# Optimization experiments

Measured on AMD Instinct MI355X. Metric: run time of the kernel, lower is better.

The kernel has to match this reference:

```python
import jax, jax.numpy as jnp
import numpy as np

LOG2PI = float(np.log(2.0 * np.pi))
CLIP_LO, CLIP_HI = 1e-6, 1.0 - 1e-6


def gaussian_log_prob(X, mu):
    # X: (s, d), mu: (K, d) -> (s, K); unit-variance diagonal Normal.
    d = X.shape[-1]
    sq = (
        (X * X).sum(-1, keepdims=True)
        - 2.0 * (X @ mu.T)
        + (mu * mu).sum(-1)[None, :]
    )
    return -0.5 * (sq + d * LOG2PI)


def setup_inputs() -> dict:
    key = jax.random.key(0)
    kz, ks, kd, km1, km2 = jax.random.split(key, 5)
    s, K, n, dz = 60000, 200, 6, 64
    Z = jax.random.normal(kz, (s, dz), dtype=jnp.float32)
    S = jax.random.normal(ks, (s, 3), dtype=jnp.float32)
    D = jax.random.randint(kd, (s, n), 0, s, dtype=jnp.int64)
    sel_mu = jax.random.normal(km1, (K, dz), dtype=jnp.float32)
    spa_mu = jax.random.normal(km2, (K, 3), dtype=jnp.float32)
    return {"Z": Z, "S": S, "D": D, "sel_mu": sel_mu, "spa_mu": spa_mu}


def reference(Z, S, D, sel_mu, spa_mu):
    # point energy U: (s, K)
    U = -(gaussian_log_prob(Z, sel_mu) + gaussian_log_prob(S, spa_mu))
    Q = jax.nn.softmax(-U, axis=-1)  # temperature = 1.0
    # expected point energy: (s,)
    point = (Q * U).sum(-1)
    # doublet energy: gather neighbor rows, coassignment, potential, mask
    Qc = jnp.clip(Q, CLIP_LO, CLIP_HI)
    co = jnp.einsum('snk,sk->sn', Qc[D], Qc)  # (s, n)
    doublet = jnp.where(D < 0, 0.0, -jnp.log(co)).sum(-1)  # (s,)
    return point + doublet
```

## Files before the change

### kernel.cpp

```cpp
#include <hip/hip_runtime.h>
#include <hip/hip_fp16.h>
#include <math.h>

#define KK 200
#define NT 13
#define NNB 6
#define Q8STRIDE 256

typedef __attribute__((ext_vector_type(8))) short short8;
typedef __attribute__((ext_vector_type(4))) float f32x4;
typedef _Float16 half2v __attribute__((ext_vector_type(2)));
typedef __fp16 fp16x2 __attribute__((ext_vector_type(2)));
#define MFMA16 __builtin_amdgcn_mfma_f32_16x16x32_bf16

union U8 { short8 s; uint4 u; };
union H2U { half2v h; unsigned u; };
union P2U { fp16x2 h; unsigned u; };

__device__ __forceinline__ unsigned short bfh(float f) {
    unsigned u = __float_as_uint(f);
    return (unsigned short)((u + 0x7fffu + ((u >> 16) & 1u)) >> 16);
}
__device__ __forceinline__ float bf2f(unsigned short h) {
    return __uint_as_float(((unsigned)h) << 16);
}
__device__ __forceinline__ short8 z8() {
    short8 v;
#pragma unroll
    for (int j = 0; j < 8; ++j) v[j] = 0;
    return v;
}
__device__ __forceinline__ void cvp(float f0, float f1, unsigned& hw, unsigned& lw) {
    unsigned u0 = __float_as_uint(f0), u1 = __float_as_uint(f1);
    float l0 = f0 - __uint_as_float(u0 & 0xffff0000u);
    float l1 = f1 - __uint_as_float(u1 & 0xffff0000u);
    hw = __builtin_amdgcn_perm(u1, u0, 0x07060302u);
    lw = __builtin_amdgcn_perm(__float_as_uint(l1), __float_as_uint(l0), 0x07060302u);
}
__device__ __forceinline__ unsigned e5pair_lo(unsigned w) {
    return __builtin_amdgcn_perm(w, 0u, 0x05000400u);
}
__device__ __forceinline__ unsigned e5pair_hi(unsigned w) {
    return __builtin_amdgcn_perm(w, 0u, 0x07000600u);
}
__device__ __forceinline__ half2v as_h2(unsigned u) { H2U x; x.u = u; return x.h; }
__device__ __forceinline__ unsigned pkrtz_u(float a, float b) {
    P2U x; x.h = __builtin_amdgcn_cvt_pkrtz(a, b); return x.u;
}

__global__ __launch_bounds__(512, 4) void
k_point(const float* __restrict__ Z, const float* __restrict__ S,
        const float* __restrict__ selmu, const float* __restrict__ spamu,
        unsigned char* __restrict__ Qc8, float* __restrict__ pointbuf,
        int sRows, int mTiles)
{
    __shared__ short8 ldsBh[26 * 64];
    __shared__ short8 ldsBl[26 * 64];
    __shared__ uint2  ldsB2h[NT * 16];
    __shared__ uint2  ldsB2l[NT * 16];
    __shared__ float  normAcc[NT * 16];

    const int tid = threadIdx.x;

    if (tid < NT * 16) normAcc[tid] = 0.f;
    __syncthreads();

    for (int slot = tid; slot < 26 * 64; slot += 512) {
        int L = slot & 63, ts = slot >> 6;
        int t = ts >> 1, sstep = ts & 1;
        int n = t * 16 + (L & 15);
        int kb = sstep * 32 + (L >> 4) * 8;
        U8 hi, lo;
        hi.s = z8(); lo.s = z8();
        if (n < KK) {
            const float* mp = selmu + (size_t)n * 64 + kb;
            float4 a = *(const float4*)mp;
            float4 b = *(const float4*)(mp + 4);
            cvp(a.x, a.y, hi.u.x, lo.u.x);
            cvp(a.z, a.w, hi.u.y, lo.u.y);
            cvp(b.x, b.y, hi.u.z, lo.u.z);
            cvp(b.z, b.w, hi.u.w, lo.u.w);
            float ss = a.x*a.x + a.y*a.y + a.z*a.z + a.w*a.w
                     + b.x*b.x + b.y*b.y + b.z*b.z + b.w*b.w;
            atomicAdd(&normAcc[n], ss);
        }
        ldsBh[slot] = hi.s;
        ldsBl[slot] = lo.s;
    }
    __syncthreads();
    if (tid < NT * 16) {
        int n = tid;
        uint2 vh = make_uint2(0, 0), vl = make_uint2(0, 0);
        if (n < KK) {
            float p0 = spamu[n * 3 + 0], p1 = spamu[n * 3 + 1], p2 = spamu[n * 3 + 2];
            float nrm = -0.5f * (normAcc[n] + p0 * p0 + p1 * p1 + p2 * p2);
            unsigned short h0 = bfh(p0), h1 = bfh(p1), h2 = bfh(p2), h3 = bfh(nrm);
            unsigned short g0 = bfh(p0 - bf2f(h0)), g1 = bfh(p1 - bf2f(h1));
            unsigned short g2 = bfh(p2 - bf2f(h2)), g3 = bfh(nrm - bf2f(h3));
            vh = make_uint2((unsigned)h0 | ((unsigned)h1 << 16), (unsigned)h2 | ((unsigned)h3 << 16));
            vl = make_uint2((unsigned)g0 | ((unsigned)g1 << 16), (unsigned)g2 | ((unsigned)g3 << 16));
        }
        ldsB2h[tid] = vh;
        ldsB2l[tid] = vl;
    }
    __syncthreads();

    const int wave = tid >> 6;
    const int lane = tid & 63;
    const int q = lane >> 4;
    const int li = lane & 15;
    const float cLog = 0.5f * 67.0f * 1.8378770664093453f;

    const int tile = blockIdx.x * 8 + wave;
    if (tile >= mTiles) return;
    const int m0 = tile * 16;
    const int row = m0 + li;
    const int rowA = (row < sRows) ? row : (sRows - 1);

    const float* zr = Z + (size_t)rowA * 64 + q * 8;
    float4 z0 = *(const float4*)zr;
    float4 z1 = *(const float4*)(zr + 4);
    float4 z2 = *(const float4*)(zr + 32);
    float4 z3 = *(const float4*)(zr + 36);
    U8 ah0, al0, ah1, al1;
    cvp(z0.x, z0.y, ah0.u.x, al0.u.x);
    cvp(z0.z, z0.w, ah0.u.y, al0.u.y);
    cvp(z1.x, z1.y, ah0.u.z, al0.u.z);
    cvp(z1.z, z1.w, ah0.u.w, al0.u.w);
    cvp(z2.x, z2.y, ah1.u.x, al1.u.x);
    cvp(z2.z, z2.w, ah1.u.y, al1.u.y);
    cvp(z3.x, z3.y, ah1.u.z, al1.u.z);
    cvp(z3.z, z3.w, ah1.u.w, al1.u.w);

    float zz = z0.x*z0.x + z0.y*z0.y + z0.z*z0.z + z0.w*z0.w
             + z1.x*z1.x + z1.y*z1.y + z1.z*z1.z + z1.w*z1.w
             + z2.x*z2.x + z2.y*z2.y + z2.z*z2.z + z2.w*z2.w
             + z3.x*z3.x + z3.y*z3.y + z3.z*z3.z + z3.w*z3.w;
    zz += __shfl_xor(zz, 16);
    zz += __shfl_xor(zz, 32);

    float s0v = S[(size_t)rowA * 3 + 0];
    float s1v = S[(size_t)rowA * 3 + 1];
    float s2v = S[(size_t)rowA * 3 + 2];
    float cz = 0.5f * (zz + s0v * s0v + s1v * s1v + s2v * s2v) + cLog;

    U8 rsh, rsl;
    rsh.s = z8(); rsl.s = z8();
    if (lane < 16) {
        cvp(s0v, s1v, rsh.u.x, rsl.u.x);
        unsigned hw, lw;
        cvp(s2v, 1.0f, hw, lw);
        rsh.u.y = hw;
        rsl.u.y = lw & 0x0000ffffu;
    }

    f32x4 acc[NT];
#pragma unroll
    for (int t = 0; t < NT; ++t) { f32x4 zv = {0.f, 0.f, 0.f, 0.f}; acc[t] = zv; }

#pragma unroll
    for (int t = 0; t < NT; ++t) {
        short8 b0 = ldsBh[(t * 2 + 0) * 64 + lane];
        short8 b1 = ldsBh[(t * 2 + 1) * 64 + lane];
        short8 c0 = ldsBl[(t * 2 + 0) * 64 + lane];
        short8 c1 = ldsBl[(t * 2 + 1) * 64 + lane];
        uint2 bh2 = make_uint2(0, 0), bl2 = make_uint2(0, 0);
        if (lane < 16) { bh2 = ldsB2h[t * 16 + lane]; bl2 = ldsB2l[t * 16 + lane]; }
        U8 cmh, cml;
        cmh.s = z8(); cml.s = z8();
        cmh.u.x = bh2.x; cmh.u.y = bh2.y;
        cml.u.x = bl2.x; cml.u.y = bl2.y;

        acc[t] = MFMA16(b0, ah0.s, acc[t], 0, 0, 0);
        acc[t] = MFMA16(b1, ah1.s, acc[t], 0, 0, 0);
        acc[t] = MFMA16(b0, al0.s, acc[t], 0, 0, 0);
        acc[t] = MFMA16(b1, al1.s, acc[t], 0, 0, 0);
        acc[t] = MFMA16(c0, ah0.s, acc[t], 0, 0, 0);
        acc[t] = MFMA16(c1, ah1.s, acc[t], 0, 0, 0);
        acc[t] = MFMA16(cmh.s, rsh.s, acc[t], 0, 0, 0);
        acc[t] = MFMA16(cmh.s, rsl.s, acc[t], 0, 0, 0);
        acc[t] = MFMA16(cml.s, rsh.s, acc[t], 0, 0, 0);
    }

    const bool padQ = (q >= 2);
    float mx = -1e30f;
#pragma unroll
    for (int t = 0; t < NT; ++t) {
#pragma unroll
        for (int r = 0; r < 4; ++r) {
            float v = acc[t][r];
            if (t == 12 && padQ) v = -1e30f;
            acc[t][r] = v;
            mx = fmaxf(mx, v);
        }
    }
    mx = fmaxf(mx, __shfl_xor(mx, 16));
    mx = fmaxf(mx, __shfl_xor(mx, 32));
    float sl = 0.f, pl = 0.f;
#pragma unroll
    for (int t = 0; t < NT; ++t) {
#pragma unroll
        for (int r = 0; r < 4; ++r) {
            float v = acc[t][r];
            float ee = __expf(v - mx);
            sl += ee;
            pl = fmaf(ee, v, pl);
            acc[t][r] = ee;
        }
    }
    sl += __shfl_xor(sl, 16);
    sl += __shfl_xor(sl, 32);
    pl += __shfl_xor(pl, 16);
    pl += __shfl_xor(pl, 32);
    float inv = 1.0f / sl;

    if (row < sRows) {
        unsigned char* qp = Qc8 + (size_t)row * Q8STRIDE + q * 4;
#pragma unroll
        for (int t = 0; t < NT; ++t) {
            unsigned w = 0;
            if (t < 12 || !padQ) {
                float c0 = fminf(fmaxf(acc[t][0] * inv, 1e-6f), 1.0f - 1e-6f) * 1024.0f;
                float c1 = fminf(fmaxf(acc[t][1] * inv, 1e-6f), 1.0f - 1e-6f) * 1024.0f;
                float c2 = fminf(fmaxf(acc[t][2] * inv, 1e-6f), 1.0f - 1e-6f) * 1024.0f;
                float c3 = fminf(fmaxf(acc[t][3] * inv, 1e-6f), 1.0f - 1e-6f) * 1024.0f;
                unsigned ua = pkrtz_u(c0, c1);
                unsigned ub = pkrtz_u(c2, c3);
                unsigned t0 = ua + 0x007f007fu + ((ua >> 8) & 0x00010001u);
                unsigned t1 = ub + 0x007f007fu + ((ub >> 8) & 0x00010001u);
                w = __builtin_amdgcn_perm(t1, t0, 0x07050301u);
            }
            *(unsigned*)(qp + t * 16) = w;
        }
        if (lane < 16) pointbuf[row] = cz - pl * inv;
    }
}

__global__ __launch_bounds__(512, 8) void
k_doublet(const unsigned char* __restrict__ Qc8, const float* __restrict__ pointbuf,
          const int* __restrict__ D, float* __restrict__ out, int sRows)
{
    const int wave = threadIdx.x >> 6;
    const int lane = threadIdx.x & 63;
    const int half = lane >> 5;
    const int l = lane & 31;
    const int row = blockIdx.x * 8 + wave;
    if (row >= sRows) return;

    const bool act = (l < 25);
    const int lc = act ? l : 0;
    const float LN2_20 = 13.862943611198906f;

    const int* dp = D + (size_t)row * NNB;
    int da0 = dp[0], da1 = dp[1], da2 = dp[2], da3 = dp[3], da4 = dp[4], da5 = dp[5];
    int dj[3];
    dj[0] = half ? da1 : da0;
    dj[1] = half ? da3 : da2;
    dj[2] = half ? da5 : da4;

    uint2 ow = *(const uint2*)(Qc8 + (size_t)row * Q8STRIDE + lc * 8);
    uint2 nb[3];
#pragma unroll
    for (int i = 0; i < 3; ++i) {
        int dd = (dj[i] >= 0) ? dj[i] : row;
        nb[i] = *(const uint2*)(Qc8 + (size_t)dd * Q8STRIDE + lc * 8);
    }

    unsigned o0 = e5pair_lo(ow.x), o1 = e5pair_hi(ow.x);
    unsigned o2 = e5pair_lo(ow.y), o3 = e5pair_hi(ow.y);

    float pj[3];
#pragma unroll
    for (int i = 0; i < 3; ++i) {
        unsigned b0 = e5pair_lo(nb[i].x), b1 = e5pair_hi(nb[i].x);
        unsigned b2 = e5pair_lo(nb[i].y), b3 = e5pair_hi(nb[i].y);
        float t = 0.f;
#if __has_builtin(__builtin_amdgcn_fdot2)
        t = __builtin_amdgcn_fdot2(as_h2(o0), as_h2(b0), t, false);
        t = __builtin_amdgcn_fdot2(as_h2(o1), as_h2(b1), t, false);
        t = __builtin_amdgcn_fdot2(as_h2(o2), as_h2(b2), t, false);
        t = __builtin_amdgcn_fdot2(as_h2(o3), as_h2(b3), t, false);
#else
        {
            half2v ov[4] = { as_h2(o0), as_h2(o1), as_h2(o2), as_h2(o3) };
            half2v bv[4] = { as_h2(b0), as_h2(b1), as_h2(b2), as_h2(b3) };
#pragma unroll
            for (int k = 0; k < 4; ++k) {
                t = fmaf((float)ov[k][0], (float)bv[k][0], t);
                t = fmaf((float)ov[k][1], (float)bv[k][1], t);
            }
        }
#endif
        pj[i] = act ? t : 0.f;
    }
#pragma unroll
    for (int off = 1; off <= 16; off <<= 1) {
#pragma unroll
        for (int i = 0; i < 3; ++i) pj[i] += __shfl_xor(pj[i], off);
    }
    float dbl = 0.f;
#pragma unroll
    for (int i = 0; i < 3; ++i)
        if (dj[i] >= 0) dbl += LN2_20 - __logf(pj[i]);
    dbl += __shfl_xor(dbl, 32);

    if (lane == 0) out[row] = pointbuf[row] + dbl;
}

extern "C" void kernel_launch(void* const* d_in, const int* in_sizes, int n_in,
                              void* d_out, int out_size, void* d_ws, size_t ws_size,
                              hipStream_t stream) {
    const float* Z     = (const float*)d_in[0];
    const float* S     = (const float*)d_in[1];
    const int*   D     = (const int*)d_in[2];
    const float* selmu = (const float*)d_in[3];
    const float* spamu = (const float*)d_in[4];
    float* out = (float*)d_out;
    const int s = out_size;

    unsigned char* Qc8 = (unsigned char*)d_ws;
    float* pointbuf = (float*)((char*)d_ws + (size_t)s * Q8STRIDE);

    const int mTiles = (s + 15) / 16;
    const int grid1 = (mTiles + 7) / 8;
    k_point<<<grid1, 512, 0, stream>>>(Z, S, selmu, spamu, Qc8, pointbuf, s, mTiles);

    const int grid2 = (s + 7) / 8;
    k_doublet<<<grid2, 512, 0, stream>>>(Qc8, pointbuf, D, out, s);
}
```

Before: 103.8 us.

## Map one doublet row per 16-lane group with 16-byte loads and DPP reduction

```diff
diff --git a/kernel.cpp b/kernel.cpp
--- a/kernel.cpp
+++ b/kernel.cpp
@@ -47,6 +47,9 @@
 __device__ __forceinline__ unsigned pkrtz_u(float a, float b) {
     P2U x; x.h = __builtin_amdgcn_cvt_pkrtz(a, b); return x.u;
 }
+#define DPP_ROR_ADD(t, ctrl)                                                        \
+    t += __int_as_float(__builtin_amdgcn_update_dpp(0, __float_as_int(t), (ctrl),   \
+                                                    0xF, 0xF, true))
 
 __global__ __launch_bounds__(512, 4) void
 k_point(const float* __restrict__ Z, const float* __restrict__ S,
@@ -232,6 +235,9 @@
             }
             *(unsigned*)(qp + t * 16) = w;
         }
+        *(unsigned*)(qp + 13 * 16) = 0u;
+        *(unsigned*)(qp + 14 * 16) = 0u;
+        *(unsigned*)(qp + 15 * 16) = 0u;
         if (lane < 16) pointbuf[row] = cz - pl * inv;
     }
 }
@@ -240,71 +246,71 @@
 k_doublet(const unsigned char* __restrict__ Qc8, const float* __restrict__ pointbuf,
           const int* __restrict__ D, float* __restrict__ out, int sRows)
 {
+    const int lane = threadIdx.x & 63;
     const int wave = threadIdx.x >> 6;
-    const int lane = threadIdx.x & 63;
-    const int half = lane >> 5;
-    const int l = lane & 31;
-    const int row = blockIdx.x * 8 + wave;
+    const int g = lane >> 4;
+    const int l16 = lane & 15;
+    const int row = blockIdx.x * 32 + wave * 4 + g;
     if (row >= sRows) return;
 
-    const bool act = (l < 25);
-    const int lc = act ? l : 0;
     const float LN2_20 = 13.862943611198906f;
 
     const int* dp = D + (size_t)row * NNB;
-    int da0 = dp[0], da1 = dp[1], da2 = dp[2], da3 = dp[3], da4 = dp[4], da5 = dp[5];
-    int dj[3];
-    dj[0] = half ? da1 : da0;
-    dj[1] = half ? da3 : da2;
-    dj[2] = half ? da5 : da4;
-
-    uint2 ow = *(const uint2*)(Qc8 + (size_t)row * Q8STRIDE + lc * 8);
-    uint2 nb[3];
-#pragma unroll
-    for (int i = 0; i < 3; ++i) {
-        int dd = (dj[i] >= 0) ? dj[i] : row;
-        nb[i] = *(const uint2*)(Qc8 + (size_t)dd * Q8STRIDE + lc * 8);
+    int2 d01 = *(const int2*)dp;
+    int2 d23 = *(const int2*)(dp + 2);
+    int2 d45 = *(const int2*)(dp + 4);
+    const int dj[6] = { d01.x, d01.y, d23.x, d23.y, d45.x, d45.y };
+
+    const unsigned off = (unsigned)l16 * 16u;
+    uint4 ow = *(const uint4*)(Qc8 + (size_t)row * Q8STRIDE + off);
+    uint4 nb[NNB];
+#pragma unroll
+    for (int j = 0; j < NNB; ++j) {
+        int dd = (dj[j] >= 0) ? dj[j] : row;
+        nb[j] = *(const uint4*)(Qc8 + (size_t)dd * Q8STRIDE + off);
     }
 
     unsigned o0 = e5pair_lo(ow.x), o1 = e5pair_hi(ow.x);
     unsigned o2 = e5pair_lo(ow.y), o3 = e5pair_hi(ow.y);
-
-    float pj[3];
-#pragma unroll
-    for (int i = 0; i < 3; ++i) {
-        unsigned b0 = e5pair_lo(nb[i].x), b1 = e5pair_hi(nb[i].x);
-        unsigned b2 = e5pair_lo(nb[i].y), b3 = e5pair_hi(nb[i].y);
+    unsigned o4 = e5pair_lo(ow.z), o5 = e5pair_hi(ow.z);
+    unsigned o6 = e5pair_lo(ow.w), o7 = e5pair_hi(ow.w);
+
+    float dbl = 0.f;
+#pragma unroll
+    for (int j = 0; j < NNB; ++j) {
         float t = 0.f;
 #if __has_builtin(__builtin_amdgcn_fdot2)
-        t = __builtin_amdgcn_fdot2(as_h2(o0), as_h2(b0), t, false);
-        t = __builtin_amdgcn_fdot2(as_h2(o1), as_h2(b1), t, false);
-        t = __builtin_amdgcn_fdot2(as_h2(o2), as_h2(b2), t, false);
-        t = __builtin_amdgcn_fdot2(as_h2(o3), as_h2(b3), t, false);
+        t = __builtin_amdgcn_fdot2(as_h2(o0), as_h2(e5pair_lo(nb[j].x)), t, false);
+        t = __builtin_amdgcn_fdot2(as_h2(o1), as_h2(e5pair_hi(nb[j].x)), t, false);
+        t = __builtin_amdgcn_fdot2(as_h2(o2), as_h2(e5pair_lo(nb[j].y)), t, false);
+        t = __builtin_amdgcn_fdot2(as_h2(o3), as_h2(e5pair_hi(nb[j].y)), t, false);
+        t = __builtin_amdgcn_fdot2(as_h2(o4), as_h2(e5pair_lo(nb[j].z)), t, false);
+        t = __builtin_amdgcn_fdot2(as_h2(o5), as_h2(e5pair_hi(nb[j].z)), t, false);
+        t = __builtin_amdgcn_fdot2(as_h2(o6), as_h2(e5pair_lo(nb[j].w)), t, false);
+        t = __builtin_amdgcn_fdot2(as_h2(o7), as_h2(e5pair_hi(nb[j].w)), t, false);
 #else
         {
-            half2v ov[4] = { as_h2(o0), as_h2(o1), as_h2(o2), as_h2(o3) };
-            half2v bv[4] = { as_h2(b0), as_h2(b1), as_h2(b2), as_h2(b3) };
-#pragma unroll
-            for (int k = 0; k < 4; ++k) {
-                t = fmaf((float)ov[k][0], (float)bv[k][0], t);
-                t = fmaf((float)ov[k][1], (float)bv[k][1], t);
+            unsigned ov[8] = { o0, o1, o2, o3, o4, o5, o6, o7 };
+            unsigned bv[8] = { e5pair_lo(nb[j].x), e5pair_hi(nb[j].x),
+                               e5pair_lo(nb[j].y), e5pair_hi(nb[j].y),
+                               e5pair_lo(nb[j].z), e5pair_hi(nb[j].z),
+                               e5pair_lo(nb[j].w), e5pair_hi(nb[j].w) };
+#pragma unroll
+            for (int k = 0; k < 8; ++k) {
+                half2v a = as_h2(ov[k]), b = as_h2(bv[k]);
+                t = fmaf((float)a[0], (float)b[0], t);
+                t = fmaf((float)a[1], (float)b[1], t);
             }
         }
 #endif
-        pj[i] = act ? t : 0.f;
-    }
-#pragma unroll
-    for (int off = 1; off <= 16; off <<= 1) {
-#pragma unroll
-        for (int i = 0; i < 3; ++i) pj[i] += __shfl_xor(pj[i], off);
-    }
-    float dbl = 0.f;
-#pragma unroll
-    for (int i = 0; i < 3; ++i)
-        if (dj[i] >= 0) dbl += LN2_20 - __logf(pj[i]);
-    dbl += __shfl_xor(dbl, 32);
-
-    if (lane == 0) out[row] = pointbuf[row] + dbl;
+        DPP_ROR_ADD(t, 0x128);
+        DPP_ROR_ADD(t, 0x124);
+        DPP_ROR_ADD(t, 0x122);
+        DPP_ROR_ADD(t, 0x121);
+        if (dj[j] >= 0) dbl += LN2_20 - __logf(t);
+    }
+
+    if (l16 == 0) out[row] = pointbuf[row] + dbl;
 }
 
 extern "C" void kernel_launch(void* const* d_in, const int* in_sizes, int n_in,
@@ -325,6 +331,6 @@
     const int grid1 = (mTiles + 7) / 8;
     k_point<<<grid1, 512, 0, stream>>>(Z, S, selmu, spamu, Qc8, pointbuf, s, mTiles);
 
-    const int grid2 = (s + 7) / 8;
+    const int grid2 = (s + 31) / 32;
     k_doublet<<<grid2, 512, 0, stream>>>(Qc8, pointbuf, D, out, s);
 }
```

Result: faster. 101.7 us (median of 2 runs) (-2.1%).
